# Optimization experiments

Hardware: AMD Instinct MI355X
Metric: run time of the kernel (lower is better)

The kernel has to match this reference:

```python
import jax, jax.numpy as jnp
import numpy as np


def setup_inputs() -> dict:
    key = jax.random.key(0)
    ks = jax.random.split(key, 7)
    B, T, X, H, Y = 256, 2048, 64, 128, 32
    s_ih = 1.0 / np.sqrt(H)
    return {
        "x": jax.random.normal(ks[0], (B, T, X), dtype=jnp.float32),
        "W_ih": jax.random.normal(ks[1], (H, X), dtype=jnp.float32) * s_ih,
        "W_hh": jax.random.normal(ks[2], (H, H), dtype=jnp.float32) * s_ih,
        "b_ih": jax.random.normal(ks[3], (H,), dtype=jnp.float32) * s_ih,
        "b_hh": jax.random.normal(ks[4], (H,), dtype=jnp.float32) * s_ih,
        "W_out": jax.random.normal(ks[5], (Y, H), dtype=jnp.float32) * s_ih,
        "b_out": jax.random.normal(ks[6], (Y,), dtype=jnp.float32) * s_ih,
    }


def reference(x, W_ih, W_hh, b_ih, b_hh, W_out, b_out):
    # Vanilla tanh RNN (torch.nn.RNN, 1 layer, batch_first), zero initial state,
    # readout on the last timestep: h_t = tanh(x_t W_ih^T + b_ih + h_{t-1} W_hh^T + b_hh)
    B, T, X = x.shape
    H = W_hh.shape[0]
    # Precompute input projections for all timesteps in one big GEMM: [T, B, H]
    xs = (jnp.einsum('bti,hi->bth', x, W_ih) + (b_ih + b_hh)).transpose(1, 0, 2)

    def step(h, xt):
        h = jnp.tanh(xt + h @ W_hh.T)
        return h, None

    h0 = jnp.zeros((B, H), dtype=x.dtype)
    h_last, _ = jax.lax.scan(step, h0, xs)
    out = h_last @ W_out.T + b_out  # [B, Y]
    return out
```

## Files before the change

kernel.cpp:

```cpp
#include <hip/hip_runtime.h>

#define TT 2048
#define BB 256
#define XX 64
#define HH 128
#define YY 32
#define SSTR 20
#define HBUF (8 * SSTR)


typedef float v2f __attribute__((ext_vector_type(2)));
typedef float v4f __attribute__((ext_vector_type(4)));

#define PKFMA(acc, a, b)                                              \
    asm("v_pk_fma_f32 %0, %1, %2, %0 op_sel:[0,0,0] op_sel_hi:[1,1,1]"\
        : "+v"(acc) : "v"(a), "v"(b))

template<int CTRL>
static __device__ __forceinline__ float dpp_mov(float s) {
    return __int_as_float(__builtin_amdgcn_update_dpp(
        0, __float_as_int(s), CTRL, 0xF, 0xF, true));
}

static __device__ __forceinline__ void pin2(v2f& v) {
    asm volatile("" : "+v"(v));
}

#define LO2(v) __builtin_shufflevector(v, v, 0, 1)
#define HI2(v) __builtin_shufflevector(v, v, 2, 3)

__global__ __launch_bounds__(512)
__attribute__((amdgpu_waves_per_eu(2, 2)))
void rnn_persist_kernel(const float* __restrict__ x,
                        const float* __restrict__ W_ih,
                        const float* __restrict__ W_hh,
                        const float* __restrict__ b_ih,
                        const float* __restrict__ b_hh,
                        const float* __restrict__ W_out,
                        const float* __restrict__ b_out,
                        float* __restrict__ out)
{
    __shared__ __align__(16) float h_lds[2][HBUF];

    const int tid  = threadIdx.x;
    const int b    = blockIdx.x;
    const int w    = tid >> 6;
    const int lane = tid & 63;
    const int kg   = (lane & 3) | ((lane >> 1) & 4);
    const int jgl  = ((lane >> 2) & 1) | (((lane >> 4) & 3) << 1);
    const int jg   = w * 8 + jgl;
    const int j0   = jg * 2;
    const int b0   = lane & 1;
    const bool writer = (lane & 10) == 0;

    const float SC = 2.8853900817779268f;

    v2f whh2[2][8];
    v2f wih2[2][4];
    float bs[2];
    #pragma unroll
    for (int jj = 0; jj < 2; ++jj) {
        const v2f* ph = (const v2f*)(W_hh + (j0 + jj) * HH + kg * 16);
        #pragma unroll
        for (int c = 0; c < 8; ++c) whh2[jj][c] = ph[c] * SC;
        const v2f* pi = (const v2f*)(W_ih + (j0 + jj) * XX + kg * 8);
        #pragma unroll
        for (int c = 0; c < 4; ++c) wih2[jj][c] = pi[c] * SC;
        bs[jj] = (b_ih[j0 + jj] + b_hh[j0 + jj]) * SC;
    }
    #pragma unroll
    for (int jj = 0; jj < 2; ++jj) {
        #pragma unroll
        for (int c = 0; c < 8; ++c) pin2(whh2[jj][c]);
        #pragma unroll
        for (int c = 0; c < 4; ++c) pin2(wih2[jj][c]);
    }
    const float bsel = b0 ? bs[1] : bs[0];

    const int jw   = j0 + b0;
    const int woff = (jw >> 4) * SSTR + (jw & 15);

    const float* xg = x + (size_t)b * TT * XX + kg * 8;

    if (tid < HBUF) h_lds[0][tid] = 0.f;

    v4f xa0 = ((const v4f*)xg)[0];
    v4f xa1 = ((const v4f*)xg)[1];
    v4f xb0 = ((const v4f*)(xg + XX))[0];
    v4f xb1 = ((const v4f*)(xg + XX))[1];
    __syncthreads();

#define STEP(RP, WP, X0, X1)                                              \
    do {                                                                  \
        const v4f* hp = (const v4f*)&h_lds[RP][kg * SSTR];                \
        const v4f H0 = hp[0], H1 = hp[1], H2 = hp[2], H3 = hp[3];         \
        const v2f h2[8] = { LO2(H0), HI2(H0), LO2(H1), HI2(H1),           \
                            LO2(H2), HI2(H2), LO2(H3), HI2(H3) };         \
        const v2f x2[4] = { LO2(X0), HI2(X0), LO2(X1), HI2(X1) };         \
        float s[2];                                                       \
        _Pragma("unroll")                                                 \
        for (int jj = 0; jj < 2; ++jj) {                                  \
            v2f a = {0.f, 0.f}, c = {0.f, 0.f};                           \
            PKFMA(a, wih2[jj][0], x2[0]); PKFMA(c, wih2[jj][1], x2[1]);   \
            PKFMA(a, wih2[jj][2], x2[2]); PKFMA(c, wih2[jj][3], x2[3]);   \
            PKFMA(a, whh2[jj][0], h2[0]); PKFMA(c, whh2[jj][1], h2[1]);   \
            PKFMA(a, whh2[jj][2], h2[2]); PKFMA(c, whh2[jj][3], h2[3]);   \
            PKFMA(a, whh2[jj][4], h2[4]); PKFMA(c, whh2[jj][5], h2[5]);   \
            PKFMA(a, whh2[jj][6], h2[6]); PKFMA(c, whh2[jj][7], h2[7]);   \
            a = a + c;                                                    \
            s[jj] = a.x + a.y;                                            \
        }                                                                 \
        \
        float u = b0 ? s[1] : s[0];            \
        float v = b0 ? s[0] : s[1];            \
        u += dpp_mov<0xB1>(v);            \
        u += dpp_mov<0x4E>(u);            \
        u += dpp_mov<0x128>(u);         \
        u += bsel;                         \
        const float e  = __builtin_amdgcn_exp2f(u);                       \
        const float hn = fmaf(-2.f, __builtin_amdgcn_rcpf(e + 1.f), 1.f); \
        if (writer) h_lds[WP][woff] = hn;                                 \
        __syncthreads();                                                  \
    } while (0)

    for (int t = 0; t < TT; t += 2) {
        STEP(0, 1, xa0, xa1);
        {
            const int tn = (t + 2 < TT) ? t + 2 : TT - 1;
            const v4f* xp = (const v4f*)(xg + (size_t)tn * XX);
            xa0 = xp[0]; xa1 = xp[1];
        }
        STEP(1, 0, xb0, xb1);
        {
            const int tn = (t + 3 < TT) ? t + 3 : TT - 1;
            const v4f* xp = (const v4f*)(xg + (size_t)tn * XX);
            xb0 = xp[0]; xb1 = xp[1];
        }
    }
#undef STEP

    if (tid < YY) {
        const float* h  = h_lds[0];
        const float* wr = W_out + tid * HH;
        float r0 = 0.f, r1 = 0.f, r2 = 0.f, r3 = 0.f;
        #pragma unroll
        for (int s8 = 0; s8 < 8; ++s8) {
            #pragma unroll
            for (int c = 0; c < 4; ++c) {
                const float4 wv = *(const float4*)(wr + s8 * 16 + c * 4);
                const float4 hv = *(const float4*)(h + s8 * SSTR + c * 4);
                r0 = fmaf(wv.x, hv.x, r0); r1 = fmaf(wv.y, hv.y, r1);
                r2 = fmaf(wv.z, hv.z, r2); r3 = fmaf(wv.w, hv.w, r3);
            }
        }
        out[b * YY + tid] = b_out[tid] + ((r0 + r1) + (r2 + r3));
    }
}

extern "C" void kernel_launch(void* const* d_in, const int* in_sizes, int n_in,
                              void* d_out, int out_size, void* d_ws, size_t ws_size,
                              hipStream_t stream) {
    const float* x     = (const float*)d_in[0];
    const float* W_ih  = (const float*)d_in[1];
    const float* W_hh  = (const float*)d_in[2];
    const float* b_ih  = (const float*)d_in[3];
    const float* b_hh  = (const float*)d_in[4];
    const float* W_out = (const float*)d_in[5];
    const float* b_out = (const float*)d_in[6];
    float* out = (float*)d_out;

    rnn_persist_kernel<<<BB, 512, 0, stream>>>(x, W_ih, W_hh, b_ih, b_hh,
                                               W_out, b_out, out);
}
```

Baseline: 590.0 us.

## Load one float4 of h per lane and rotate across quad with DPP

Each lane now reads a single v4f of the hidden state from LDS and obtains the other three quad chunks by DPP quad rotations instead of four LDS vector loads per step. The padded LDS stride goes away, the weight layout is permuted to match the rotation order, and the cross-lane reduction now uses DPP, ds_swizzle and permlane32_swap over 8 k-groups instead of a quad DPP reduce. The aim is less LDS traffic and latency on the serial recurrence critical path, at the cost of extra DPP ops and a ds_swizzle, which goes through the LDS unit, in the reduction.

```diff
diff --git a/kernel.cpp b/kernel.cpp
--- a/kernel.cpp
+++ b/kernel.cpp
@@ -5,8 +5,6 @@
 #define XX 64
 #define HH 128
 #define YY 32
-#define SSTR 20
-#define HBUF (8 * SSTR)
 
 
 typedef float v2f __attribute__((ext_vector_type(2)));
@@ -20,6 +18,15 @@
 static __device__ __forceinline__ float dpp_mov(float s) {
     return __int_as_float(__builtin_amdgcn_update_dpp(
         0, __float_as_int(s), CTRL, 0xF, 0xF, true));
+}
+
+static __device__ __forceinline__ v4f rot_quad(v4f h) {
+    v4f r;
+    r.x = dpp_mov<0x39>(h.x);
+    r.y = dpp_mov<0x39>(h.y);
+    r.z = dpp_mov<0x39>(h.z);
+    r.w = dpp_mov<0x39>(h.w);
+    return r;
 }
 
 static __device__ __forceinline__ void pin2(v2f& v) {
@@ -40,49 +47,48 @@
                         const float* __restrict__ b_out,
                         float* __restrict__ out)
 {
-    __shared__ __align__(16) float h_lds[2][HBUF];
+    __shared__ __align__(16) float h_lds[2][HH];
 
     const int tid  = threadIdx.x;
     const int b    = blockIdx.x;
     const int w    = tid >> 6;
     const int lane = tid & 63;
-    const int kg   = (lane & 3) | ((lane >> 1) & 4);
-    const int jgl  = ((lane >> 2) & 1) | (((lane >> 4) & 3) << 1);
-    const int jg   = w * 8 + jgl;
-    const int j0   = jg * 2;
-    const int b0   = lane & 1;
-    const bool writer = (lane & 10) == 0;
+    const int l2   = lane & 3;
+    const int jh   = (lane >> 2) & 1;
+    const int mk   = lane >> 3;
+    const int o    = mk & 1;
+    const int jA   = w * 16 + jh * 8 + l2;
+    const int jB   = jA + 4;
 
     const float SC = 2.8853900817779268f;
 
-    v2f whh2[2][8];
-    v2f wih2[2][4];
-    float bs[2];
+    v2f wa[8], wb[8];
+    v2f wia[4], wib[4];
     #pragma unroll
-    for (int jj = 0; jj < 2; ++jj) {
-        const v2f* ph = (const v2f*)(W_hh + (j0 + jj) * HH + kg * 16);
+    for (int r = 0; r < 4; ++r) {
+        const int ch = (l2 + r) & 3;
+        const v2f* pa = (const v2f*)(W_hh + jA * HH + 16 * mk + 4 * ch);
+        const v2f* pb = (const v2f*)(W_hh + jB * HH + 16 * mk + 4 * ch);
+        wa[2*r] = pa[0] * SC; wa[2*r+1] = pa[1] * SC;
+        wb[2*r] = pb[0] * SC; wb[2*r+1] = pb[1] * SC;
+    }
+    {
+        const v2f* pia = (const v2f*)(W_ih + jA * XX + 8 * mk);
+        const v2f* pib = (const v2f*)(W_ih + jB * XX + 8 * mk);
         #pragma unroll
-        for (int c = 0; c < 8; ++c) whh2[jj][c] = ph[c] * SC;
-        const v2f* pi = (const v2f*)(W_ih + (j0 + jj) * XX + kg * 8);
-        #pragma unroll
-        for (int c = 0; c < 4; ++c) wih2[jj][c] = pi[c] * SC;
-        bs[jj] = (b_ih[j0 + jj] + b_hh[j0 + jj]) * SC;
+        for (int c = 0; c < 4; ++c) { wia[c] = pia[c] * SC; wib[c] = pib[c] * SC; }
     }
     #pragma unroll
-    for (int jj = 0; jj < 2; ++jj) {
-        #pragma unroll
-        for (int c = 0; c < 8; ++c) pin2(whh2[jj][c]);
-        #pragma unroll
-        for (int c = 0; c < 4; ++c) pin2(wih2[jj][c]);
-    }
-    const float bsel = b0 ? bs[1] : bs[0];
+    for (int c = 0; c < 8; ++c) { pin2(wa[c]); pin2(wb[c]); }
+    #pragma unroll
+    for (int c = 0; c < 4; ++c) { pin2(wia[c]); pin2(wib[c]); }
 
-    const int jw   = j0 + b0;
-    const int woff = (jw >> 4) * SSTR + (jw & 15);
+    const float bsel = (o ? (b_ih[jB] + b_hh[jB]) : (b_ih[jA] + b_hh[jA])) * SC;
+    const int   jwr  = w * 16 + jh * 8 + o * 4 + l2;
 
-    const float* xg = x + (size_t)b * TT * XX + kg * 8;
+    const float* xg = x + (size_t)b * TT * XX + 8 * mk;
 
-    if (tid < HBUF) h_lds[0][tid] = 0.f;
+    if (tid < HH) h_lds[0][tid] = 0.f;
 
     v4f xa0 = ((const v4f*)xg)[0];
     v4f xa1 = ((const v4f*)xg)[1];
@@ -90,37 +96,47 @@
     v4f xb1 = ((const v4f*)(xg + XX))[1];
     __syncthreads();
 
-#define STEP(RP, WP, X0, X1)                                              \
-    do {                                                                  \
-        const v4f* hp = (const v4f*)&h_lds[RP][kg * SSTR];                \
-        const v4f H0 = hp[0], H1 = hp[1], H2 = hp[2], H3 = hp[3];         \
-        const v2f h2[8] = { LO2(H0), HI2(H0), LO2(H1), HI2(H1),           \
-                            LO2(H2), HI2(H2), LO2(H3), HI2(H3) };         \
-        const v2f x2[4] = { LO2(X0), HI2(X0), LO2(X1), HI2(X1) };         \
-        float s[2];                                                       \
-        _Pragma("unroll")                                                 \
-        for (int jj = 0; jj < 2; ++jj) {                                  \
-            v2f a = {0.f, 0.f}, c = {0.f, 0.f};                           \
-            PKFMA(a, wih2[jj][0], x2[0]); PKFMA(c, wih2[jj][1], x2[1]);   \
-            PKFMA(a, wih2[jj][2], x2[2]); PKFMA(c, wih2[jj][3], x2[3]);   \
-            PKFMA(a, whh2[jj][0], h2[0]); PKFMA(c, whh2[jj][1], h2[1]);   \
-            PKFMA(a, whh2[jj][2], h2[2]); PKFMA(c, whh2[jj][3], h2[3]);   \
-            PKFMA(a, whh2[jj][4], h2[4]); PKFMA(c, whh2[jj][5], h2[5]);   \
-            PKFMA(a, whh2[jj][6], h2[6]); PKFMA(c, whh2[jj][7], h2[7]);   \
-            a = a + c;                                                    \
-            s[jj] = a.x + a.y;                                            \
-        }                                                                 \
-        \
-        float u = b0 ? s[1] : s[0];            \
-        float v = b0 ? s[0] : s[1];            \
-        u += dpp_mov<0xB1>(v);            \
-        u += dpp_mov<0x4E>(u);            \
-        u += dpp_mov<0x128>(u);         \
-        u += bsel;                         \
-        const float e  = __builtin_amdgcn_exp2f(u);                       \
+#define STEP(RP, WP, X0, X1)                                               \
+    do {                                                                   \
+        v4f hc = *(const v4f*)&h_lds[RP][16 * mk + 4 * l2];                \
+        v2f aA = {0.f,0.f}, aA2 = {0.f,0.f};                               \
+        v2f aB = {0.f,0.f}, aB2 = {0.f,0.f};                               \
+                \
+        PKFMA(aA, wia[0], LO2(X0)); PKFMA(aA2, wia[1], HI2(X0));           \
+        PKFMA(aA, wia[2], LO2(X1)); PKFMA(aA2, wia[3], HI2(X1));           \
+        PKFMA(aB, wib[0], LO2(X0)); PKFMA(aB2, wib[1], HI2(X0));           \
+        PKFMA(aB, wib[2], LO2(X1)); PKFMA(aB2, wib[3], HI2(X1));           \
+                                                    \
+        PKFMA(aA, wa[0], LO2(hc)); PKFMA(aA2, wa[1], HI2(hc));             \
+        PKFMA(aB, wb[0], LO2(hc)); PKFMA(aB2, wb[1], HI2(hc));             \
+        hc = rot_quad(hc);                                                 \
+        PKFMA(aA, wa[2], LO2(hc)); PKFMA(aA2, wa[3], HI2(hc));             \
+        PKFMA(aB, wb[2], LO2(hc)); PKFMA(aB2, wb[3], HI2(hc));             \
+        hc = rot_quad(hc);                                                 \
+        PKFMA(aA, wa[4], LO2(hc)); PKFMA(aA2, wa[5], HI2(hc));             \
+        PKFMA(aB, wb[4], LO2(hc)); PKFMA(aB2, wb[5], HI2(hc));             \
+        hc = rot_quad(hc);                                                 \
+        PKFMA(aA, wa[6], LO2(hc)); PKFMA(aA2, wa[7], HI2(hc));             \
+        PKFMA(aB, wb[6], LO2(hc)); PKFMA(aB2, wb[7], HI2(hc));             \
+        aA = aA + aA2; aB = aB + aB2;                                      \
+        const float sA = aA.x + aA.y;                                      \
+        const float sB = aB.x + aB.y;                                      \
+             \
+        float u  = o ? sB : sA;                                            \
+        float vv = o ? sA : sB;                                            \
+        u += dpp_mov<0x128>(vv);                     \
+        u += __int_as_float(__builtin_amdgcn_ds_swizzle(                   \
+                 __float_as_int(u), 0x401F));                   \
+        {                                                                  \
+            float pa_ = u, pb_ = u;                                        \
+            asm("v_permlane32_swap_b32 %0, %1" : "+v"(pa_), "+v"(pb_));    \
+            u = pa_ + pb_;                                      \
+        }                                                                  \
+        u += bsel;                               \
+        const float e  = __builtin_amdgcn_exp2f(u);                        \
         const float hn = fmaf(-2.f, __builtin_amdgcn_rcpf(e + 1.f), 1.f); \
-        if (writer) h_lds[WP][woff] = hn;                                 \
-        __syncthreads();                                                  \
+        if (lane < 16) h_lds[WP][jwr] = hn;                                \
+        __syncthreads();                                                   \
     } while (0)
 
     for (int t = 0; t < TT; t += 2) {
@@ -144,14 +160,11 @@
         const float* wr = W_out + tid * HH;
         float r0 = 0.f, r1 = 0.f, r2 = 0.f, r3 = 0.f;
         #pragma unroll
-        for (int s8 = 0; s8 < 8; ++s8) {
-            #pragma unroll
-            for (int c = 0; c < 4; ++c) {
-                const float4 wv = *(const float4*)(wr + s8 * 16 + c * 4);
-                const float4 hv = *(const float4*)(h + s8 * SSTR + c * 4);
-                r0 = fmaf(wv.x, hv.x, r0); r1 = fmaf(wv.y, hv.y, r1);
-                r2 = fmaf(wv.z, hv.z, r2); r3 = fmaf(wv.w, hv.w, r3);
-            }
+        for (int c = 0; c < 32; ++c) {
+            const float4 wv = *(const float4*)(wr + c * 4);
+            const float4 hv = *(const float4*)(h + c * 4);
+            r0 = fmaf(wv.x, hv.x, r0); r1 = fmaf(wv.y, hv.y, r1);
+            r2 = fmaf(wv.z, hv.z, r2); r3 = fmaf(wv.w, hv.w, r3);
         }
         out[b * YY + tid] = b_out[tid] + ((r0 + r1) + (r2 + r3));
     }
```

Result: slower. 760.1 us (+28.8%).
